# Performance work log

Hardware: AMD Instinct MI355X
Metric: run time of the kernel (lower is better)

The kernel has to match this reference:

```python
import jax, jax.numpy as jnp
import numpy as np

N, T, D, H = 8192, 128, 64, 512  # batch, time grid len, latent dim, ode_func hidden


def setup_inputs() -> dict:
    key = jax.random.key(0)
    ks = jax.random.split(key, 6)
    hxs = jax.random.normal(ks[0], (N, D), dtype=jnp.float32)
    # PPO-style done masks in {0,1}, shape [N,1]
    masks = (jax.random.uniform(ks[1], (N, 1)) > 0.1).astype(jnp.float32)
    # strictly increasing per-sample time grids; t0 > 0 so every sample integrates
    dts = 0.01 + 0.02 * jax.random.uniform(ks[2], (N, T), dtype=jnp.float32)
    time_steps = jnp.cumsum(dts, axis=1)
    # ode_func: 2-layer tanh MLP, dh/dt = tanh(h W1 + b1) W2 + b2
    W1 = jax.random.normal(ks[3], (D, H), dtype=jnp.float32) / np.float32(np.sqrt(D))
    b1 = jnp.zeros((H,), jnp.float32)
    W2 = jax.random.normal(ks[4], (H, D), dtype=jnp.float32) / np.float32(np.sqrt(H))
    b2 = jnp.zeros((D,), jnp.float32)
    return {"time_steps": time_steps, "hxs": hxs, "masks": masks,
            "W1": W1, "b1": b1, "W2": W2, "b2": b2}


def reference(time_steps, hxs, masks, W1, b1, W2, b2):
    # first_point = (hxs * masks); torchdiffeq explicit_adams (Adams-Bashforth,
    # fixed grid, order<=4 with lower-order startup) integrated per sample over
    # its own time grid, returning the state at the final time. Vectorized over N.
    first_point = hxs * masks                        # [N, D]
    f = lambda y: jnp.tanh(y @ W1 + b1) @ W2 + b2    # autonomous ode_func

    dt = (time_steps[:, 1:] - time_steps[:, :-1]).T  # [T-1, N]
    f0 = f(first_point)

    def step(carry, inp):
        y, f1, f2, f3 = carry        # f1=f_{n-1}, f2=f_{n-2}, f3=f_{n-3}
        dt_n, j = inp                # dt_n: [N], j: step index
        fn = f(y)                    # one RHS eval per step (AB is explicit)
        inc1 = fn                                    # AB1 (Euler)
        inc2 = (3.0 * fn - f1) * 0.5                 # AB2
        inc3 = (23.0 * fn - 16.0 * f1 + 5.0 * f2) / 12.0   # AB3
        inc4 = (55.0 * fn - 59.0 * f1 + 37.0 * f2 - 9.0 * f3) / 24.0  # AB4
        inc = jnp.where(j < 1, inc1,
              jnp.where(j < 2, inc2,
              jnp.where(j < 3, inc3, inc4)))
        y_next = y + dt_n[:, None] * inc
        return (y_next, fn, f1, f2), None

    init = (first_point, f0, f0, f0)
    steps = jnp.arange(time_steps.shape[1] - 1)
    (y_final, _, _, _), _ = jax.lax.scan(step, init, (dt, steps))

    # samples whose first time is exactly 0 pass first_point through unchanged
    pred = jnp.where(time_steps[:, :1] == 0.0, first_point, y_final)  # [N, D]
    return pred
```

## Files before the change

### kernel.cpp

```cpp
#include <hip/hip_runtime.h>


#define NS 8192
#define TT 128
#define DD 64
#define HH 512
#define BM 16
#define NSTEP (TT - 1)

typedef _Float16 half8 __attribute__((ext_vector_type(8)));
typedef _Float16 half4 __attribute__((ext_vector_type(4)));
typedef __fp16 fp16x2 __attribute__((ext_vector_type(2)));
typedef float f32x4 __attribute__((ext_vector_type(4)));


__global__ __launch_bounds__(256) void prep_weights(
    const float* __restrict__ W1, const float* __restrict__ W2,
    _Float16* __restrict__ wsp) {
  int idx = blockIdx.x * 256 + threadIdx.x;
  if (idx < HH * DD) {
    int d = idx / HH, j = idx % HH;
    wsp[j * DD + d] = (_Float16)W1[idx];
  } else {
    int k = idx - HH * DD;
    int j = k / DD, d = k % DD;
    wsp[HH * DD + d * HH + j] = (_Float16)W2[k];
  }
}

__device__ __forceinline__ float fast_tanh(float x) {
  float e = __builtin_amdgcn_exp2f(-2.8853900817779268f * fabsf(x));
  float r = (1.0f - e) * __builtin_amdgcn_rcpf(1.0f + e);
  return copysignf(r, x);
}

__device__ __forceinline__ half4 pack4(float a, float b, float c2, float d) {
  fp16x2 lo = __builtin_amdgcn_cvt_pkrtz(a, b);
  fp16x2 hi = __builtin_amdgcn_cvt_pkrtz(c2, d);
  half4 r;
  r[0] = (_Float16)lo[0]; r[1] = (_Float16)lo[1];
  r[2] = (_Float16)hi[0]; r[3] = (_Float16)hi[1];
  return r;
}

__global__ __launch_bounds__(512, 4) void ode_mfma_kernel(
    const float* __restrict__ ts, const float* __restrict__ hxs,
    const float* __restrict__ masks, const float* __restrict__ b1,
    const float* __restrict__ b2, const _Float16* __restrict__ wsp,
    float* __restrict__ out) {
  __shared__ __align__(16) _Float16 Zh[BM][520];
  __shared__ __align__(16) _Float16 Yh[BM][72];
  __shared__ __align__(16) float DTs[BM][129];
  __shared__ __align__(16) float Pb[4][64][4];

  const int t = threadIdx.x;
  const int w = t >> 6, l = t & 63;
  const int c = l & 15, q = l >> 4;
  const int m0 = blockIdx.x * BM;
  const int db = w >> 1, ks = w & 1;
  const int m = c;
  const int d0 = db * 16 + 4 * q;

  const _Float16* W1Th = wsp;
  const _Float16* W2Th = wsp + HH * DD;

  half8 w1h[4][2];
#pragma unroll
  for (int jl = 0; jl < 4; ++jl)
#pragma unroll
    for (int kk = 0; kk < 2; ++kk) {
      int off = ((4 * w + jl) * 16 + c) * DD + kk * 32 + 8 * q;
      w1h[jl][kk] = *(const half8*)&W1Th[off];
    }
  half8 w2h[8];
#pragma unroll
  for (int kkl = 0; kkl < 8; ++kkl) {
    int kg = ks * 8 + kkl;
    w2h[kkl] = *(const half8*)&W2Th[(db * 16 + c) * HH + kg * 32 + 8 * q];
  }

  f32x4 b1f[4];
#pragma unroll
  for (int jl = 0; jl < 4; ++jl)
    b1f[jl] = *(const f32x4*)&b1[(4 * w + jl) * 16 + 4 * q];
  const f32x4 b2v = *(const f32x4*)&b2[d0];

  for (int idx = t; idx < BM * TT; idx += 512) {
    int mm = idx >> 7, s = idx & (TT - 1);
    float v = 0.0f;
    if (s < NSTEP) v = ts[(m0 + mm) * TT + s + 1] - ts[(m0 + mm) * TT + s];
    DTs[mm][s] = v;
  }

  float y[4], f1[4], f2[4], f3[4];
  if (ks == 0) {
    const float mk = masks[m0 + m];
    f32x4 y0 = *(const f32x4*)&hxs[(m0 + m) * DD + d0];
#pragma unroll
    for (int r = 0; r < 4; ++r) {
      y[r] = y0[r] * mk;
      f1[r] = f2[r] = f3[r] = 0.0f;
    }
    *(half4*)&Yh[m][d0] = pack4(y[0], y[1], y[2], y[3]);
  }
  __syncthreads();

  for (int s = 0; s < NSTEP; ++s) {
    {
      half8 yh[2];
#pragma unroll
      for (int kk = 0; kk < 2; ++kk)
        yh[kk] = *(const half8*)&Yh[c][kk * 32 + 8 * q];
#pragma unroll
      for (int jl = 0; jl < 4; ++jl) {
        f32x4 acc = b1f[jl];
        __builtin_amdgcn_s_setprio(1);
#pragma unroll
        for (int kk = 0; kk < 2; ++kk)
          acc = __builtin_amdgcn_mfma_f32_16x16x32_f16(w1h[jl][kk], yh[kk], acc, 0, 0, 0);
        __builtin_amdgcn_s_setprio(0);
        *(half4*)&Zh[c][(4 * w + jl) * 16 + 4 * q] =
            pack4(fast_tanh(acc[0]), fast_tanh(acc[1]),
                  fast_tanh(acc[2]), fast_tanh(acc[3]));
      }
    }
    __syncthreads();

    f32x4 acc = {0.0f, 0.0f, 0.0f, 0.0f};
    __builtin_amdgcn_s_setprio(1);
#pragma unroll
    for (int kkl = 0; kkl < 8; ++kkl) {
      const int kg = ks * 8 + kkl;
      half8 zh = *(const half8*)&Zh[m][kg * 32 + 8 * q];
      acc = __builtin_amdgcn_mfma_f32_16x16x32_f16(w2h[kkl], zh, acc, 0, 0, 0);
    }
    __builtin_amdgcn_s_setprio(0);
    if (ks == 1) {
      *(f32x4*)&Pb[db][l][0] = acc;
    }
    __syncthreads();

    if (ks == 0) {
      const f32x4 po = *(const f32x4*)&Pb[db][l][0];
      const float dtv = DTs[m][s];
#pragma unroll
      for (int r = 0; r < 4; ++r) {
        float fn = acc[r] + po[r] + b2v[r];
        float inc;
        if (s == 0)      inc = fn;
        else if (s == 1) inc = (3.0f * fn - f1[r]) * 0.5f;
        else if (s == 2) inc = (23.0f * fn - 16.0f * f1[r] + 5.0f * f2[r]) * (1.0f / 12.0f);
        else             inc = (55.0f * fn - 59.0f * f1[r] + 37.0f * f2[r] - 9.0f * f3[r]) * (1.0f / 24.0f);
        y[r] += dtv * inc;
        f3[r] = f2[r]; f2[r] = f1[r]; f1[r] = fn;
      }
      *(half4*)&Yh[m][d0] = pack4(y[0], y[1], y[2], y[3]);
    }
    __syncthreads();
  }

  if (ks == 0) {
    const float mk = masks[m0 + m];
    float ts0 = ts[(m0 + m) * TT];
    f32x4 o;
    if (ts0 == 0.0f) {
      f32x4 h4 = *(const f32x4*)&hxs[(m0 + m) * DD + d0];
#pragma unroll
      for (int r = 0; r < 4; ++r) o[r] = h4[r] * mk;
    } else {
#pragma unroll
      for (int r = 0; r < 4; ++r) o[r] = y[r];
    }
    *(f32x4*)&out[(m0 + m) * DD + d0] = o;
  }
}

extern "C" void kernel_launch(void* const* d_in, const int* in_sizes, int n_in,
                              void* d_out, int out_size, void* d_ws, size_t ws_size,
                              hipStream_t stream) {
  const float* ts    = (const float*)d_in[0];
  const float* hxs   = (const float*)d_in[1];
  const float* masks = (const float*)d_in[2];
  const float* W1    = (const float*)d_in[3];
  const float* b1    = (const float*)d_in[4];
  const float* W2    = (const float*)d_in[5];
  const float* b2    = (const float*)d_in[6];
  float* out = (float*)d_out;
  _Float16* wsp = (_Float16*)d_ws;
  (void)in_sizes; (void)n_in; (void)out_size; (void)ws_size;

  prep_weights<<<dim3((2 * HH * DD) / 256), dim3(256), 0, stream>>>(W1, W2, wsp);
  ode_mfma_kernel<<<dim3(NS / BM), dim3(512), 0, stream>>>(ts, hxs, masks, b1, b2, wsp, out);
}
```

Baseline: 287.7 us.

## Double rows per block and split second GEMM by row instead of K

Each block now processes 32 samples instead of 16. Each wave pair owns a 16-row half for the second matmul and the state update, replacing the K-split with its partial-sum exchange through shared memory and the extra barrier per step. This removes one __syncthreads and the LDS reduction per step, and lets all waves do the AB update instead of half of them. In exchange it doubles first-layer MFMA work per wave, doubles W2 register residency, halves the block count to 256, and lowers the occupancy hint to 2 blocks.

Result: slower. 304.4 us (+5.8%).

```diff
diff --git a/kernel.cpp b/kernel.cpp
--- a/kernel.cpp
+++ b/kernel.cpp
@@ -5,7 +5,7 @@
 #define TT 128
 #define DD 64
 #define HH 512
-#define BM 16
+#define BM 32
 #define NSTEP (TT - 1)
 
 typedef _Float16 half8 __attribute__((ext_vector_type(8)));
@@ -43,7 +43,7 @@
   return r;
 }
 
-__global__ __launch_bounds__(512, 4) void ode_mfma_kernel(
+__global__ __launch_bounds__(512, 2) void ode_mfma_kernel(
     const float* __restrict__ ts, const float* __restrict__ hxs,
     const float* __restrict__ masks, const float* __restrict__ b1,
     const float* __restrict__ b2, const _Float16* __restrict__ wsp,
@@ -51,14 +51,13 @@
   __shared__ __align__(16) _Float16 Zh[BM][520];
   __shared__ __align__(16) _Float16 Yh[BM][72];
   __shared__ __align__(16) float DTs[BM][129];
-  __shared__ __align__(16) float Pb[4][64][4];
 
   const int t = threadIdx.x;
   const int w = t >> 6, l = t & 63;
   const int c = l & 15, q = l >> 4;
   const int m0 = blockIdx.x * BM;
-  const int db = w >> 1, ks = w & 1;
-  const int m = c;
+  const int db = w >> 1, mb = w & 1;
+  const int m = mb * 16 + c;
   const int d0 = db * 16 + 4 * q;
 
   const _Float16* W1Th = wsp;
@@ -72,12 +71,10 @@
       int off = ((4 * w + jl) * 16 + c) * DD + kk * 32 + 8 * q;
       w1h[jl][kk] = *(const half8*)&W1Th[off];
     }
-  half8 w2h[8];
+  half8 w2h[16];
 #pragma unroll
-  for (int kkl = 0; kkl < 8; ++kkl) {
-    int kg = ks * 8 + kkl;
-    w2h[kkl] = *(const half8*)&W2Th[(db * 16 + c) * HH + kg * 32 + 8 * q];
-  }
+  for (int kg = 0; kg < 16; ++kg)
+    w2h[kg] = *(const half8*)&W2Th[(db * 16 + c) * HH + kg * 32 + 8 * q];
 
   f32x4 b1f[4];
 #pragma unroll
@@ -93,7 +90,7 @@
   }
 
   float y[4], f1[4], f2[4], f3[4];
-  if (ks == 0) {
+  {
     const float mk = masks[m0 + m];
     f32x4 y0 = *(const f32x4*)&hxs[(m0 + m) * DD + d0];
 #pragma unroll
@@ -106,11 +103,12 @@
   __syncthreads();
 
   for (int s = 0; s < NSTEP; ++s) {
-    {
+#pragma unroll
+    for (int mbt = 0; mbt < 2; ++mbt) {
       half8 yh[2];
 #pragma unroll
       for (int kk = 0; kk < 2; ++kk)
-        yh[kk] = *(const half8*)&Yh[c][kk * 32 + 8 * q];
+        yh[kk] = *(const half8*)&Yh[mbt * 16 + c][kk * 32 + 8 * q];
 #pragma unroll
       for (int jl = 0; jl < 4; ++jl) {
         f32x4 acc = b1f[jl];
@@ -119,7 +117,7 @@
         for (int kk = 0; kk < 2; ++kk)
           acc = __builtin_amdgcn_mfma_f32_16x16x32_f16(w1h[jl][kk], yh[kk], acc, 0, 0, 0);
         __builtin_amdgcn_s_setprio(0);
-        *(half4*)&Zh[c][(4 * w + jl) * 16 + 4 * q] =
+        *(half4*)&Zh[mbt * 16 + c][(4 * w + jl) * 16 + 4 * q] =
             pack4(fast_tanh(acc[0]), fast_tanh(acc[1]),
                   fast_tanh(acc[2]), fast_tanh(acc[3]));
       }
@@ -129,23 +127,17 @@
     f32x4 acc = {0.0f, 0.0f, 0.0f, 0.0f};
     __builtin_amdgcn_s_setprio(1);
 #pragma unroll
-    for (int kkl = 0; kkl < 8; ++kkl) {
-      const int kg = ks * 8 + kkl;
+    for (int kg = 0; kg < 16; ++kg) {
       half8 zh = *(const half8*)&Zh[m][kg * 32 + 8 * q];
-      acc = __builtin_amdgcn_mfma_f32_16x16x32_f16(w2h[kkl], zh, acc, 0, 0, 0);
+      acc = __builtin_amdgcn_mfma_f32_16x16x32_f16(w2h[kg], zh, acc, 0, 0, 0);
     }
     __builtin_amdgcn_s_setprio(0);
-    if (ks == 1) {
-      *(f32x4*)&Pb[db][l][0] = acc;
-    }
-    __syncthreads();
 
-    if (ks == 0) {
-      const f32x4 po = *(const f32x4*)&Pb[db][l][0];
+    {
       const float dtv = DTs[m][s];
 #pragma unroll
       for (int r = 0; r < 4; ++r) {
-        float fn = acc[r] + po[r] + b2v[r];
+        float fn = acc[r] + b2v[r];
         float inc;
         if (s == 0)      inc = fn;
         else if (s == 1) inc = (3.0f * fn - f1[r]) * 0.5f;
@@ -159,7 +151,7 @@
     __syncthreads();
   }
 
-  if (ks == 0) {
+  {
     const float mk = masks[m0 + m];
     float ts0 = ts[(m0 + m) * TT];
     f32x4 o;
```
